# Kernel optimization log

Measured on AMD Instinct MI355X. Metric: run time of the kernel, lower is better.

## Reference

```python
import jax, jax.numpy as jnp
import numpy as np

NUM_ATLAS = 100000
FD = 16
FS = 9  # fsize + 1
NV, NB = 65536, 8


def setup_inputs() -> dict:
    key = jax.random.key(0)
    k1, k2, k3 = jax.random.split(key, 3)
    x = jax.random.uniform(k1, (NV, NB, 2), minval=-1.0, maxval=1.0, dtype=jnp.float32)
    inds = jax.random.randint(k2, (NV, NB), 0, NUM_ATLAS)
    ft = jax.random.normal(k3, (NUM_ATLAS, FD, FS, FS), dtype=jnp.float32) * 0.1
    return {"x": x, "inds": inds, "ft": ft}


def reference(x, inds, ft):
    # Fused equivalent of: ft[inds] -> (Nv*Nb, fd, fs, fs) then
    # F.grid_sample(..., align_corners=True, padding_mode='border') at one point.
    # We index the 4 bilinear corners directly in the atlas (no big gather).
    fs = ft.shape[-1]
    # grid coords: x[...,0] -> width (last axis), x[...,1] -> height
    # align_corners=True: pix = (c + 1) / 2 * (fs - 1); border padding == clamp
    gx = jnp.clip((x[..., 0] + 1.0) * 0.5 * (fs - 1), 0.0, fs - 1.0)
    gy = jnp.clip((x[..., 1] + 1.0) * 0.5 * (fs - 1), 0.0, fs - 1.0)
    x0f = jnp.floor(gx)
    y0f = jnp.floor(gy)
    wx = (gx - x0f)[..., None]  # (Nv, Nb, 1)
    wy = (gy - y0f)[..., None]
    x0 = x0f.astype(jnp.int32)
    y0 = y0f.astype(jnp.int32)
    x1 = jnp.minimum(x0 + 1, fs - 1)
    y1 = jnp.minimum(y0 + 1, fs - 1)
    # advanced indexing with a slice in the middle -> (Nv, Nb, fd)
    v00 = ft[inds, :, y0, x0]
    v01 = ft[inds, :, y0, x1]
    v10 = ft[inds, :, y1, x0]
    v11 = ft[inds, :, y1, x1]
    top = v00 * (1.0 - wx) + v01 * wx
    bot = v10 * (1.0 - wx) + v11 * wx
    return top * (1.0 - wy) + bot * wy  # (Nv, Nb, fd)
```

## Files before the change

### kernel.cpp

```cpp
#include <hip/hip_runtime.h>


constexpr int FD = 16;
constexpr int FS = 9;
constexpr int NSAMP = 65536 * 8;
constexpr int CH_PER_THREAD = 4;
constexpr int THREADS_TOTAL = NSAMP * (FD / CH_PER_THREAD);
constexpr int BLOCK = 256;

__global__ __launch_bounds__(BLOCK) void FeatureTexel_kernel(
    const float2* __restrict__ x,
    const int*    __restrict__ inds,
    const float*  __restrict__ ft,
    float4*       __restrict__ out)
{
    int tid = blockIdx.x * BLOCK + threadIdx.x;
    int s  = tid >> 2;
    int c0 = (tid & 3) * 4;

    float2 xy = x[s];
    int ind   = inds[s];

    const float fsm1 = (float)(FS - 1);
    float gx = fminf(fmaxf((xy.x + 1.0f) * 0.5f * fsm1, 0.0f), fsm1);
    float gy = fminf(fmaxf((xy.y + 1.0f) * 0.5f * fsm1, 0.0f), fsm1);

    int x0 = (int)floorf(gx);
    int y0 = (int)floorf(gy);
    x0 = min(x0, FS - 2);
    y0 = min(y0, FS - 2);
    float wx = gx - (float)x0;
    float wy = gy - (float)y0;

    float w00 = (1.0f - wx) * (1.0f - wy);
    float w01 = wx * (1.0f - wy);
    float w10 = (1.0f - wx) * wy;
    float w11 = wx * wy;

    const float* base = ft + (size_t)ind * (FD * FS * FS)
                           + (size_t)c0 * (FS * FS)
                           + y0 * FS + x0;

    float r[CH_PER_THREAD];
    #pragma unroll
    for (int i = 0; i < CH_PER_THREAD; ++i) {
        const float* p = base + i * (FS * FS);
        float v00 = p[0];
        float v01 = p[1];
        float v10 = p[FS];
        float v11 = p[FS + 1];
        r[i] = v00 * w00 + v01 * w01 + v10 * w10 + v11 * w11;
    }

    out[tid] = make_float4(r[0], r[1], r[2], r[3]);
}

extern "C" void kernel_launch(void* const* d_in, const int* in_sizes, int n_in,
                              void* d_out, int out_size, void* d_ws, size_t ws_size,
                              hipStream_t stream) {
    const float2* x    = (const float2*)d_in[0];
    const int*    inds = (const int*)d_in[1];
    const float*  ft   = (const float*)d_in[2];
    float4*       out  = (float4*)d_out;

    FeatureTexel_kernel<<<THREADS_TOTAL / BLOCK, BLOCK, 0, stream>>>(x, inds, ft, out);
}
```

Baseline: 765.3 us.

## Counting-sort samples by atlas index before bilinear gather for locality

Adds a histogram, a three-pass prefix scan and a scatter that build a permutation grouping samples by their atlas index. The gather kernel then walks samples in sorted order, so threads reading the same atlas entry run close together and can share cached lines. Output writes become scattered through the permutation. In exchange it adds several extra launches, a memset and atomic contention, and scratch space in the workspace buffer.

```diff
diff --git a/kernel.cpp b/kernel.cpp
--- a/kernel.cpp
+++ b/kernel.cpp
@@ -4,18 +4,85 @@
 constexpr int FD = 16;
 constexpr int FS = 9;
 constexpr int NSAMP = 65536 * 8;
-constexpr int CH_PER_THREAD = 4;
-constexpr int THREADS_TOTAL = NSAMP * (FD / CH_PER_THREAD);
+constexpr int NUM_ATLAS = 100000;
 constexpr int BLOCK = 256;
 
-__global__ __launch_bounds__(BLOCK) void FeatureTexel_kernel(
+constexpr int SCAN_CHUNK = 1024;
+constexpr int NUM_SCAN_BLOCKS = (NUM_ATLAS + SCAN_CHUNK - 1) / SCAN_CHUNK;
+constexpr int PARTIALS_PAD = 128;
+
+__global__ __launch_bounds__(BLOCK) void hist_kernel(const int* __restrict__ inds,
+                                                     int* __restrict__ hist) {
+    int i = blockIdx.x * BLOCK + threadIdx.x;
+    if (i < NSAMP) atomicAdd(&hist[inds[i]], 1);
+}
+
+__global__ __launch_bounds__(BLOCK) void scanA_kernel(const int* __restrict__ hist,
+                                                      int* __restrict__ offsets,
+                                                      int* __restrict__ partials) {
+    __shared__ int lds[BLOCK];
+    int t = threadIdx.x;
+    int base = blockIdx.x * SCAN_CHUNK + t * 4;
+    int v[4];
+    #pragma unroll
+    for (int j = 0; j < 4; ++j) v[j] = (base + j < NUM_ATLAS) ? hist[base + j] : 0;
+    int sum = v[0] + v[1] + v[2] + v[3];
+    lds[t] = sum;
+    __syncthreads();
+    for (int off = 1; off < BLOCK; off <<= 1) {
+        int add = (t >= off) ? lds[t - off] : 0;
+        __syncthreads();
+        lds[t] += add;
+        __syncthreads();
+    }
+    int incl = lds[t];
+    int excl = incl - sum;
+    if (t == BLOCK - 1) partials[blockIdx.x] = incl;
+    int run = excl;
+    #pragma unroll
+    for (int j = 0; j < 4; ++j) {
+        if (base + j < NUM_ATLAS) offsets[base + j] = run;
+        run += v[j];
+    }
+}
+
+__global__ void scanB_kernel(int* __restrict__ partials) {
+    if (threadIdx.x == 0) {
+        int run = 0;
+        for (int i = 0; i < NUM_SCAN_BLOCKS; ++i) {
+            int v = partials[i];
+            partials[i] = run;
+            run += v;
+        }
+    }
+}
+
+__global__ __launch_bounds__(BLOCK) void scanC_kernel(int* __restrict__ offsets,
+                                                      const int* __restrict__ partials) {
+    int i = blockIdx.x * BLOCK + threadIdx.x;
+    if (i < NUM_ATLAS) offsets[i] += partials[i / SCAN_CHUNK];
+}
+
+__global__ __launch_bounds__(BLOCK) void scatter_kernel(const int* __restrict__ inds,
+                                                        int* __restrict__ offsets,
+                                                        int* __restrict__ order) {
+    int i = blockIdx.x * BLOCK + threadIdx.x;
+    if (i < NSAMP) {
+        int ind = inds[i];
+        int pos = atomicAdd(&offsets[ind], 1);
+        order[pos] = i;
+    }
+}
+
+__global__ __launch_bounds__(BLOCK) void gather_kernel(
     const float2* __restrict__ x,
     const int*    __restrict__ inds,
     const float*  __restrict__ ft,
+    const int*    __restrict__ order,
     float4*       __restrict__ out)
 {
     int tid = blockIdx.x * BLOCK + threadIdx.x;
-    int s  = tid >> 2;
+    int s = order[tid >> 2];
     int c0 = (tid & 3) * 4;
 
     float2 xy = x[s];
@@ -41,9 +108,9 @@
                            + (size_t)c0 * (FS * FS)
                            + y0 * FS + x0;
 
-    float r[CH_PER_THREAD];
+    float r[4];
     #pragma unroll
-    for (int i = 0; i < CH_PER_THREAD; ++i) {
+    for (int i = 0; i < 4; ++i) {
         const float* p = base + i * (FS * FS);
         float v00 = p[0];
         float v01 = p[1];
@@ -52,7 +119,7 @@
         r[i] = v00 * w00 + v01 * w01 + v10 * w10 + v11 * w11;
     }
 
-    out[tid] = make_float4(r[0], r[1], r[2], r[3]);
+    out[(size_t)s * 4 + (tid & 3)] = make_float4(r[0], r[1], r[2], r[3]);
 }
 
 extern "C" void kernel_launch(void* const* d_in, const int* in_sizes, int n_in,
@@ -63,5 +130,20 @@
     const float*  ft   = (const float*)d_in[2];
     float4*       out  = (float4*)d_out;
 
-    FeatureTexel_kernel<<<THREADS_TOTAL / BLOCK, BLOCK, 0, stream>>>(x, inds, ft, out);
+    int* ws       = (int*)d_ws;
+    int* hist     = ws;
+    int* partials = hist + NUM_ATLAS;
+    int* offsets  = partials + PARTIALS_PAD;
+    int* order    = offsets + NUM_ATLAS;
+
+    hipMemsetAsync(hist, 0, (size_t)(NUM_ATLAS + PARTIALS_PAD) * sizeof(int), stream);
+
+    hist_kernel<<<(NSAMP + BLOCK - 1) / BLOCK, BLOCK, 0, stream>>>(inds, hist);
+    scanA_kernel<<<NUM_SCAN_BLOCKS, BLOCK, 0, stream>>>(hist, offsets, partials);
+    scanB_kernel<<<1, 64, 0, stream>>>(partials);
+    scanC_kernel<<<(NUM_ATLAS + BLOCK - 1) / BLOCK, BLOCK, 0, stream>>>(offsets, partials);
+    scatter_kernel<<<(NSAMP + BLOCK - 1) / BLOCK, BLOCK, 0, stream>>>(inds, offsets, order);
+
+    int gather_threads = NSAMP * 4;
+    gather_kernel<<<gather_threads / BLOCK, BLOCK, 0, stream>>>(x, inds, ft, order, out);
 }
```

Result: faster. 736.7 us (-3.7%).
